# Kernel tuning notes

Hardware: AMD Instinct MI355X
Metric: run time of the kernel (lower is better)

## Reference

```python
import jax, jax.numpy as jnp
import numpy as np

D_MODEL = 1024
NUM_HEADS = 16
DEPTH = D_MODEL // NUM_HEADS
B, S = 2, 2048


def setup_inputs() -> dict:
    key = jax.random.key(0)
    ks = jax.random.split(key, 12)
    std = 1.0 / np.sqrt(D_MODEL)
    inp = {
        "q": jax.random.normal(ks[0], (B, S, D_MODEL), dtype=jnp.float32),
        "k": jax.random.normal(ks[1], (B, S, D_MODEL), dtype=jnp.float32),
        "v": jax.random.normal(ks[2], (B, S, D_MODEL), dtype=jnp.float32),
        "mask": jax.random.randint(ks[3], (B, 1, 1, S), 0, 2, dtype=jnp.int32),
        "wq": jax.random.normal(ks[4], (D_MODEL, D_MODEL), dtype=jnp.float32) * std,
        "bq": jnp.zeros((D_MODEL,), dtype=jnp.float32),
        "wk": jax.random.normal(ks[5], (D_MODEL, D_MODEL), dtype=jnp.float32) * std,
        "bk": jnp.zeros((D_MODEL,), dtype=jnp.float32),
        "wv": jax.random.normal(ks[6], (D_MODEL, D_MODEL), dtype=jnp.float32) * std,
        "bv": jnp.zeros((D_MODEL,), dtype=jnp.float32),
        "wo": jax.random.normal(ks[7], (D_MODEL, D_MODEL), dtype=jnp.float32) * std,
        "bo": jnp.zeros((D_MODEL,), dtype=jnp.float32),
    }
    return inp


def _split_heads(x):
    # (B, S, D) -> (B, H, S, depth)
    b, s, _ = x.shape
    return x.reshape(b, s, NUM_HEADS, DEPTH).transpose(0, 2, 1, 3)


def reference(q, k, v, mask, wq, bq, wk, bk, wv, bv, wo, bo):
    qh = _split_heads(q @ wq + bq)   # (B,H,S,depth)
    kh = _split_heads(k @ wk + bk)
    vh = _split_heads(v @ wv + bv)
    scale = 1.0 / jnp.sqrt(jnp.float32(DEPTH))
    logits = jnp.einsum("bhqd,bhkd->bhqk", qh, kh) * scale  # (B,H,Sq,Sk)
    logits = logits + mask.astype(logits.dtype) * -1e9
    attn = jax.nn.softmax(logits, axis=-1)
    out = jnp.einsum("bhqk,bhkd->bhqd", attn, vh)  # (B,H,Sq,depth)
    out = out.transpose(0, 2, 1, 3).reshape(q.shape[0], -1, D_MODEL)
    return out @ wo + bo
```

## Files before the change

kernel.cpp:

```cpp
#include <hip/hip_runtime.h>
#include <hip/hip_bf16.h>
#include <stdint.h>


typedef __bf16 bf16;
typedef __bf16 bf16x8 __attribute__((ext_vector_type(8)));
typedef __bf16 bf16x4 __attribute__((ext_vector_type(4)));
typedef float  f32x4  __attribute__((ext_vector_type(4)));

#define D_MODEL 1024
#define S_LEN   2048
#define NH      16
#define DEPTH   64

#define LOG2E   1.4426950408889634f
#define QSCALE  (0.125f * LOG2E)
#define SMAX    20.0f
#define PADPEN  (-30000.0f)

__device__ __forceinline__ void gload_lds16(const void* g, void* l) {
  __builtin_amdgcn_global_load_lds(
      (__attribute__((address_space(1))) void*)g,
      (__attribute__((address_space(3))) void*)l,
      16, 0, 0);
}

__global__ __launch_bounds__(256) void setup(
    const void* __restrict__ q, const void* __restrict__ k,
    const void* __restrict__ v, const int* __restrict__ mask,
    const void* __restrict__ wq, const void* __restrict__ wk,
    const void* __restrict__ wv, const void* __restrict__ wo,
    const void* __restrict__ bq, const void* __restrict__ bk,
    const void* __restrict__ bv, const void* __restrict__ bo,
    bf16* __restrict__ wqT, bf16* __restrict__ wkT,
    bf16* __restrict__ wvT, bf16* __restrict__ woT,
    bf16* __restrict__ bqb, bf16* __restrict__ bkb,
    bf16* __restrict__ bvb, bf16* __restrict__ bob,
    bf16* __restrict__ qb, bf16* __restrict__ kb, bf16* __restrict__ vb,
    int* __restrict__ cpos, int* __restrict__ nb, int* __restrict__ flagout)
{
  const int t = threadIdx.x;
  uint32_t w = ((const uint32_t*)q)[t];
  uint32_t e = (w >> 7) & 0xFF;
  int inr = (e >= 90 && e <= 150) ? 1 : 0;
  __shared__ int flg;
  int cnt = __syncthreads_count(inr);
  if (t == 0) flg = (cnt > 160) ? 1 : 0;
  __syncthreads();
  int flag = flg;

  const int bid = blockIdx.x;
  if (bid < 2) {
    const int b = bid;
    const int lane = t & 63, wv4 = t >> 6;
    __shared__ int wsum[4];
    int vals[8], s = 0;
#pragma unroll
    for (int j = 0; j < 8; ++j) {
      vals[j] = (mask[b * S_LEN + t * 8 + j] == 0) ? 1 : 0;
      s += vals[j];
    }
    int acc = s;
    for (int off = 1; off < 64; off <<= 1) {
      int u = __shfl_up(acc, off);
      if (lane >= off) acc += u;
    }
    if (lane == 63) wsum[wv4] = acc;
    __syncthreads();
    int base = 0;
    for (int w4 = 0; w4 < 4; ++w4) base += (w4 < wv4) ? wsum[w4] : 0;
    int ex = base + acc - s;
#pragma unroll
    for (int j = 0; j < 8; ++j) {
      cpos[b * S_LEN + t * 8 + j] = vals[j] ? ex : -1;
      ex += vals[j];
    }
    if (t == 255) nb[b] = base + acc;
    if (b == 0 && t == 0) *flagout = flag;
  } else if (bid < 6) {
    const int j = bid - 2;
    const void* B; bf16* O;
    switch (j) {
      case 0:  B = bq; O = bqb; break;
      case 1:  B = bk; O = bkb; break;
      case 2:  B = bv; O = bvb; break;
      default: B = bo; O = bob; break;
    }
    const float sc = (j == 0) ? QSCALE : 1.0f;
    for (int jj = 0; jj < 4; ++jj) {
      const int i = t + jj * 256;
      const float val = flag ? (float)((const bf16*)B)[i] : ((const float*)B)[i];
      O[i] = (bf16)(val * sc);
    }
  } else if (bid < 6 + 4096) {
    const int job = bid - 6;
    const int wsel = job >> 10, rem = job & 1023;
    const void* W; bf16* T;
    switch (wsel) {
      case 0:  W = wq; T = wqT; break;
      case 1:  W = wk; T = wkT; break;
      case 2:  W = wv; T = wvT; break;
      default: W = wo; T = woT; break;
    }
    const float sc = (wsel == 0) ? QSCALE : 1.0f;
    __shared__ float tile[32][33];
    const int tx = t & 31, ty = t >> 5;
    const int x0 = (rem & 31) * 32;
    const int y0 = (rem >> 5) * 32;
    for (int i = ty; i < 32; i += 8) {
      const size_t gi = (size_t)(y0 + i) * D_MODEL + x0 + tx;
      tile[i][tx] = flag ? (float)((const bf16*)W)[gi] : ((const float*)W)[gi];
    }
    __syncthreads();
    for (int i = ty; i < 32; i += 8)
      T[(size_t)(x0 + i) * D_MODEL + y0 + tx] = (bf16)(tile[tx][i] * sc);
  } else {
    if (flag) return;
    const int job = bid - 4102;
    const int tensor = job >> 11, blk = job & 2047;
    const void* src; bf16* dst;
    switch (tensor) {
      case 0:  src = q; dst = qb; break;
      case 1:  src = k; dst = kb; break;
      default: src = v; dst = vb; break;
    }
    const size_t idx = ((size_t)blk * 256 + t) * 8;
    const float* s = (const float*)src + idx;
    f32x4 a = *(const f32x4*)(s);
    f32x4 b2 = *(const f32x4*)(s + 4);
    bf16x8 o;
    for (int i = 0; i < 4; ++i) { o[i] = (bf16)a[i]; o[4 + i] = (bf16)b2[i]; }
    *(bf16x8*)(dst + idx) = o;
  }
}

struct GArgs {
  const bf16* A;
  const void* Araw;
  const bf16* BT;
  const bf16* bias;
  void* out;
  const int* cpos;
  int mode;
};

__device__ __forceinline__ void gemm_body(const GArgs& g, int flag)
{
  const bf16* A = flag ? (const bf16*)g.Araw : g.A;

  __shared__ __align__(16) bf16 As[2][128 * 32];
  __shared__ __align__(16) bf16 Bs[2][128 * 32];
  const int tid  = threadIdx.x;
  const int wave = tid >> 6, lane = tid & 63;
  const int quad = lane >> 4, l16 = lane & 15;

  const int flat = blockIdx.y * 8 + blockIdx.x;
  const int xcd = flat & 7, pos = flat >> 3;
  const int bx = (xcd & 1) * 4 + (pos & 3);
  const int by = (xcd >> 1) * 8 + (pos >> 2);
  const int m0 = by * 128, n0 = bx * 128;

  const int wm = (wave >> 1) * 64, wn = (wave & 1) * 64;
  const int srow = lane >> 2;
  const int scol = (((lane & 3) ^ ((lane >> 3) & 3)) * 8);

  f32x4 acc[4][4] = {};

  const bf16* Ag = A    + (size_t)(m0 + wave * 32 + srow) * D_MODEL + scol;
  const bf16* Bg = g.BT + (size_t)(n0 + wave * 32 + srow) * D_MODEL + scol;
  const int lbase = (wave * 32) * 32;
  const int rsw = (quad ^ ((l16 >> 1) & 3)) * 8;

  gload_lds16(Ag,                &As[0][lbase]);
  gload_lds16(Ag + 16 * D_MODEL, &As[0][lbase + 16 * 32]);
  gload_lds16(Bg,                &Bs[0][lbase]);
  gload_lds16(Bg + 16 * D_MODEL, &Bs[0][lbase + 16 * 32]);
  __syncthreads();

  int cur = 0;
  for (int kt = 0; kt < D_MODEL; kt += 32, cur ^= 1) {
    if (kt + 32 < D_MODEL) {
      const int nxt = cur ^ 1;
      gload_lds16(Ag + kt + 32,                &As[nxt][lbase]);
      gload_lds16(Ag + kt + 32 + 16 * D_MODEL, &As[nxt][lbase + 16 * 32]);
      gload_lds16(Bg + kt + 32,                &Bs[nxt][lbase]);
      gload_lds16(Bg + kt + 32 + 16 * D_MODEL, &Bs[nxt][lbase + 16 * 32]);
    }

    bf16x8 af[4], bfv[4];
#pragma unroll
    for (int mi = 0; mi < 4; ++mi)
      af[mi] = *(const bf16x8*)(&As[cur][(wm + mi * 16 + l16) * 32 + rsw]);
#pragma unroll
    for (int ni = 0; ni < 4; ++ni)
      bfv[ni] = *(const bf16x8*)(&Bs[cur][(wn + ni * 16 + l16) * 32 + rsw]);
#pragma unroll
    for (int mi = 0; mi < 4; ++mi)
#pragma unroll
      for (int ni = 0; ni < 4; ++ni)
        acc[mi][ni] = __builtin_amdgcn_mfma_f32_16x16x32_bf16(
            af[mi], bfv[ni], acc[mi][ni], 0, 0, 0);

    __syncthreads();
  }

#pragma unroll
  for (int mi = 0; mi < 4; ++mi) {
    const int row0 = m0 + wm + mi * 16 + quad * 4;
    const int b = row0 >> 11, s = row0 & 2047;
    int cp[4];
    if (g.mode >= 2) {
#pragma unroll
      for (int r = 0; r < 4; ++r) cp[r] = g.cpos[b * S_LEN + s + r];
    }
#pragma unroll
    for (int ni = 0; ni < 4; ++ni) {
      const int col  = n0 + wn + ni * 16 + l16;
      const float bv = (float)g.bias[col];
      const int hh = col >> 6, d = col & 63;
      if (g.mode == 3) {
        bf16* base = (bf16*)g.out + (size_t)(b * NH + hh) * S_LEN * DEPTH + d;
#pragma unroll
        for (int r = 0; r < 4; ++r)
          if (cp[r] >= 0) base[(size_t)cp[r] * DEPTH] = (bf16)(acc[mi][ni][r] + bv);
      } else if (g.mode == 2) {
        bf16* base = (bf16*)g.out + ((size_t)(b * NH + hh) * DEPTH + d) * S_LEN;
#pragma unroll
        for (int r = 0; r < 4; ++r)
          if (cp[r] >= 0) base[cp[r]] = (bf16)(acc[mi][ni][r] + bv);
      } else if (g.mode == 1) {
        bf16* op = (bf16*)g.out + ((size_t)(b * NH + hh) * S_LEN + s) * DEPTH + d;
#pragma unroll
        for (int r = 0; r < 4; ++r)
          op[(size_t)r * DEPTH] = (bf16)(acc[mi][ni][r] + bv);
      } else {
        if (flag) {
          bf16* op = (bf16*)g.out + (size_t)row0 * D_MODEL + col;
#pragma unroll
          for (int r = 0; r < 4; ++r)
            op[(size_t)r * D_MODEL] = (bf16)(acc[mi][ni][r] + bv);
        } else {
          float* op = (float*)g.out + (size_t)row0 * D_MODEL + col;
#pragma unroll
          for (int r = 0; r < 4; ++r)
            op[(size_t)r * D_MODEL] = acc[mi][ni][r] + bv;
        }
      }
    }
  }
}

__global__ __launch_bounds__(256) void gemm_qkv(GArgs g0, GArgs g1, GArgs g2,
                                                const int* __restrict__ flagp)
{
  const GArgs& g = (blockIdx.z == 0) ? g0 : ((blockIdx.z == 1) ? g1 : g2);
  gemm_body(g, *flagp);
}

__global__ __launch_bounds__(256) void gemm_out(GArgs g,
                                                const int* __restrict__ flagp)
{
  gemm_body(g, *flagp);
}

__global__ __launch_bounds__(256) void attn(
    const bf16* __restrict__ Qh, const bf16* __restrict__ Kc,
    const bf16* __restrict__ Vc, const int* __restrict__ nbp,
    bf16* __restrict__ Oh)
{
  const int bh = blockIdx.y;
  const int b  = bh >> 4;
  const int h  = bh & 15;
  const int q0 = blockIdx.x * 128;
  const int tid = threadIdx.x, wave = tid >> 6, lane = tid & 63;
  const int quad = lane >> 4, l16 = lane & 15;

  __shared__ __align__(16) bf16 Ks[64][72];
  __shared__ __align__(16) bf16 Vts[64][72];
  __shared__ __align__(16) bf16 Ps[4][32][72];

  const int nbv = nbp[b];
  const int nb_pad = (nbv + 63) & ~63;

  const bf16* Qg = Qh + ((size_t)bh * S_LEN + q0 + wave * 32) * DEPTH;
  bf16x8 aq00 = *(const bf16x8*)(Qg + (size_t)l16 * DEPTH + quad * 8);
  bf16x8 aq01 = *(const bf16x8*)(Qg + (size_t)l16 * DEPTH + 32 + quad * 8);
  bf16x8 aq10 = *(const bf16x8*)(Qg + (size_t)(16 + l16) * DEPTH + quad * 8);
  bf16x8 aq11 = *(const bf16x8*)(Qg + (size_t)(16 + l16) * DEPTH + 32 + quad * 8);

  bf16x8 ones;
#pragma unroll
  for (int j = 0; j < 8; ++j) ones[j] = (bf16)1.0f;

  f32x4 o_acc[2][4] = {};
  f32x4 l_acc[2] = {};

  const bf16* Kg = Kc + (size_t)bh * S_LEN * DEPTH;
  const bf16* Vg = Vc + (size_t)bh * DEPTH * S_LEN;

  const int sr0 = tid >> 3, sc0 = (tid & 7) * 8;
  const int sr1 = sr0 + 32;

  bf16x8 kr0, kr1, vr0, vr1;
  {
    kr0 = *(const bf16x8*)(Kg + (size_t)sr0 * DEPTH + sc0);
    kr1 = *(const bf16x8*)(Kg + (size_t)sr1 * DEPTH + sc0);
    vr0 = *(const bf16x8*)(Vg + (size_t)sr0 * S_LEN + sc0);
    vr1 = *(const bf16x8*)(Vg + (size_t)sr1 * S_LEN + sc0);
  }

  for (int kb = 0; kb < nb_pad; kb += 64) {
    __syncthreads();
    *(bf16x8*)(&Ks[sr0][sc0])  = kr0;
    *(bf16x8*)(&Ks[sr1][sc0])  = kr1;
    *(bf16x8*)(&Vts[sr0][sc0]) = vr0;
    *(bf16x8*)(&Vts[sr1][sc0]) = vr1;
    __syncthreads();
    if (kb + 64 < nb_pad) {
      kr0 = *(const bf16x8*)(Kg + (size_t)(kb + 64 + sr0) * DEPTH + sc0);
      kr1 = *(const bf16x8*)(Kg + (size_t)(kb + 64 + sr1) * DEPTH + sc0);
      vr0 = *(const bf16x8*)(Vg + (size_t)sr0 * S_LEN + kb + 64 + sc0);
      vr1 = *(const bf16x8*)(Vg + (size_t)sr1 * S_LEN + kb + 64 + sc0);
    }

    f32x4 sacc[2][4] = {};
#pragma unroll
    for (int jn = 0; jn < 4; ++jn) {
      bf16x8 bk0 = *(const bf16x8*)(&Ks[jn * 16 + l16][quad * 8]);
      bf16x8 bk1 = *(const bf16x8*)(&Ks[jn * 16 + l16][32 + quad * 8]);
      sacc[0][jn] = __builtin_amdgcn_mfma_f32_16x16x32_bf16(aq00, bk0, sacc[0][jn], 0, 0, 0);
      sacc[0][jn] = __builtin_amdgcn_mfma_f32_16x16x32_bf16(aq01, bk1, sacc[0][jn], 0, 0, 0);
      sacc[1][jn] = __builtin_amdgcn_mfma_f32_16x16x32_bf16(aq10, bk0, sacc[1][jn], 0, 0, 0);
      sacc[1][jn] = __builtin_amdgcn_mfma_f32_16x16x32_bf16(aq11, bk1, sacc[1][jn], 0, 0, 0);
    }

#pragma unroll
    for (int jn = 0; jn < 4; ++jn) {
      const int key = kb + jn * 16 + l16;
      const float pen = (key < nbv) ? (-SMAX) : PADPEN;
#pragma unroll
      for (int qs = 0; qs < 2; ++qs)
#pragma unroll
        for (int r = 0; r < 4; ++r)
          Ps[wave][qs * 16 + quad * 4 + r][jn * 16 + l16] =
              (bf16)__builtin_amdgcn_exp2f(sacc[qs][jn][r] + pen);
    }

    bf16x8 ap00 = *(const bf16x8*)(&Ps[wave][l16][quad * 8]);
    bf16x8 ap01 = *(const bf16x8*)(&Ps[wave][l16][32 + quad * 8]);
    bf16x8 ap10 = *(const bf16x8*)(&Ps[wave][16 + l16][quad * 8]);
    bf16x8 ap11 = *(const bf16x8*)(&Ps[wave][16 + l16][32 + quad * 8]);
#pragma unroll
    for (int jd = 0; jd < 4; ++jd) {
      bf16x8 bv0 = *(const bf16x8*)(&Vts[jd * 16 + l16][quad * 8]);
      bf16x8 bv1 = *(const bf16x8*)(&Vts[jd * 16 + l16][32 + quad * 8]);
      o_acc[0][jd] = __builtin_amdgcn_mfma_f32_16x16x32_bf16(ap00, bv0, o_acc[0][jd], 0, 0, 0);
      o_acc[0][jd] = __builtin_amdgcn_mfma_f32_16x16x32_bf16(ap01, bv1, o_acc[0][jd], 0, 0, 0);
      o_acc[1][jd] = __builtin_amdgcn_mfma_f32_16x16x32_bf16(ap10, bv0, o_acc[1][jd], 0, 0, 0);
      o_acc[1][jd] = __builtin_amdgcn_mfma_f32_16x16x32_bf16(ap11, bv1, o_acc[1][jd], 0, 0, 0);
    }
    l_acc[0] = __builtin_amdgcn_mfma_f32_16x16x32_bf16(ap00, ones, l_acc[0], 0, 0, 0);
    l_acc[0] = __builtin_amdgcn_mfma_f32_16x16x32_bf16(ap01, ones, l_acc[0], 0, 0, 0);
    l_acc[1] = __builtin_amdgcn_mfma_f32_16x16x32_bf16(ap10, ones, l_acc[1], 0, 0, 0);
    l_acc[1] = __builtin_amdgcn_mfma_f32_16x16x32_bf16(ap11, ones, l_acc[1], 0, 0, 0);
  }

#pragma unroll
  for (int qs = 0; qs < 2; ++qs) {
#pragma unroll
    for (int r = 0; r < 4; ++r) {
      const int s = q0 + wave * 32 + qs * 16 + quad * 4 + r;
      const float inv = 1.f / l_acc[qs][r];
#pragma unroll
      for (int jd = 0; jd < 4; ++jd) {
        const int d = jd * 16 + l16;
        Oh[(size_t)(b * S_LEN + s) * D_MODEL + h * DEPTH + d] =
            (bf16)(o_acc[qs][jd][r] * inv);
      }
    }
  }
}

extern "C" void kernel_launch(void* const* d_in, const int* in_sizes, int n_in,
                              void* d_out, int out_size, void* d_ws, size_t ws_size,
                              hipStream_t stream)
{
  const void* q    = d_in[0];
  const void* k    = d_in[1];
  const void* v    = d_in[2];
  const int*  mask = (const int*)d_in[3];
  const void* wq   = d_in[4];
  const void* bq   = d_in[5];
  const void* wk   = d_in[6];
  const void* bk   = d_in[7];
  const void* wv   = d_in[8];
  const void* bv   = d_in[9];
  const void* wo   = d_in[10];
  const void* bo   = d_in[11];

  char* ws = (char*)d_ws;
  const size_t MB = 1u << 20;
  bf16* Qh  = (bf16*)(ws + 0 * MB);
  bf16* Kc  = (bf16*)(ws + 8 * MB);
  bf16* Vc  = (bf16*)(ws + 16 * MB);
  bf16* Oh  = (bf16*)(ws + 24 * MB);
  bf16* wqT = (bf16*)(ws + 32 * MB);
  bf16* wkT = (bf16*)(ws + 34 * MB);
  bf16* wvT = (bf16*)(ws + 36 * MB);
  bf16* woT = (bf16*)(ws + 38 * MB);
  bf16* bqb = (bf16*)(ws + 40 * MB);
  bf16* bkb = (bf16*)(ws + 40 * MB + 4096);
  bf16* bvb = (bf16*)(ws + 40 * MB + 8192);
  bf16* bob = (bf16*)(ws + 40 * MB + 12288);
  int*  flag = (int*)(ws + 40 * MB + 32768);
  int*  cpos = (int*)(ws + 40 * MB + 65536);
  int*  nb   = (int*)(ws + 40 * MB + 65536 + 16384);
  bf16* qb  = (bf16*)(ws + 41 * MB);
  bf16* kb_ = (bf16*)(ws + 49 * MB);
  bf16* vb_ = (bf16*)(ws + 57 * MB);

  setup<<<10246, 256, 0, stream>>>(
      q, k, v, mask, wq, wk, wv, wo, bq, bk, bv, bo,
      wqT, wkT, wvT, woT, bqb, bkb, bvb, bob,
      qb, kb_, vb_, cpos, nb, flag);

  GArgs gq{qb,  q,  wqT, bqb, Qh, nullptr, 1};
  GArgs gk{kb_, k,  wkT, bkb, Kc, cpos,    3};
  GArgs gv{vb_, v,  wvT, bvb, Vc, cpos,    2};
  gemm_qkv<<<dim3(8, 32, 3), 256, 0, stream>>>(gq, gk, gv, flag);

  attn<<<dim3(16, 32), 256, 0, stream>>>(Qh, Kc, Vc, nb, Oh);

  GArgs go{Oh, Oh, woT, bob, d_out, nullptr, 0};
  gemm_out<<<dim3(8, 32), 256, 0, stream>>>(go, flag);
}
```

Measured before the change: 232.0 us.

## Triple-buffer GEMM LDS tiles with prefetch distance two and vmcnt waits

The projection GEMM mainloop moves from a double-buffered LDS scheme to a three-stage ring that prefetches two K-tiles ahead. The full __syncthreads is replaced by an explicit s_waitcnt vmcnt plus s_barrier, so each step waits only for the oldest tile's loads. This lets global-to-LDS loads overlap more with MFMA work and removes a barrier per iteration. In exchange it uses 1.5x the shared memory, which may lower occupancy, and relies on hand-counted vmcnt values being correct.

```diff
diff --git a/kernel.cpp b/kernel.cpp
--- a/kernel.cpp
+++ b/kernel.cpp
@@ -148,8 +148,8 @@
 {
   const bf16* A = flag ? (const bf16*)g.Araw : g.A;
 
-  __shared__ __align__(16) bf16 As[2][128 * 32];
-  __shared__ __align__(16) bf16 Bs[2][128 * 32];
+  __shared__ __align__(16) bf16 As[3][128 * 32];
+  __shared__ __align__(16) bf16 Bs[3][128 * 32];
   const int tid  = threadIdx.x;
   const int wave = tid >> 6, lane = tid & 63;
   const int quad = lane >> 4, l16 = lane & 15;
@@ -171,21 +171,20 @@
   const int lbase = (wave * 32) * 32;
   const int rsw = (quad ^ ((l16 >> 1) & 3)) * 8;
 
-  gload_lds16(Ag,                &As[0][lbase]);
-  gload_lds16(Ag + 16 * D_MODEL, &As[0][lbase + 16 * 32]);
-  gload_lds16(Bg,                &Bs[0][lbase]);
-  gload_lds16(Bg + 16 * D_MODEL, &Bs[0][lbase + 16 * 32]);
-  __syncthreads();
+#pragma unroll
+  for (int p = 0; p < 2; ++p) {
+    gload_lds16(Ag + p * 32,                &As[p][lbase]);
+    gload_lds16(Ag + p * 32 + 16 * D_MODEL, &As[p][lbase + 16 * 32]);
+    gload_lds16(Bg + p * 32,                &Bs[p][lbase]);
+    gload_lds16(Bg + p * 32 + 16 * D_MODEL, &Bs[p][lbase + 16 * 32]);
+  }
 
   int cur = 0;
-  for (int kt = 0; kt < D_MODEL; kt += 32, cur ^= 1) {
-    if (kt + 32 < D_MODEL) {
-      const int nxt = cur ^ 1;
-      gload_lds16(Ag + kt + 32,                &As[nxt][lbase]);
-      gload_lds16(Ag + kt + 32 + 16 * D_MODEL, &As[nxt][lbase + 16 * 32]);
-      gload_lds16(Bg + kt + 32,                &Bs[nxt][lbase]);
-      gload_lds16(Bg + kt + 32 + 16 * D_MODEL, &Bs[nxt][lbase + 16 * 32]);
-    }
+  for (int t = 0; t < 32; ++t) {
+    if (t >= 30) asm volatile("s_waitcnt vmcnt(0)" ::: "memory");
+    else         asm volatile("s_waitcnt vmcnt(4)" ::: "memory");
+    __builtin_amdgcn_s_barrier();
+    __builtin_amdgcn_sched_barrier(0);
 
     bf16x8 af[4], bfv[4];
 #pragma unroll
@@ -201,7 +200,15 @@
         acc[mi][ni] = __builtin_amdgcn_mfma_f32_16x16x32_bf16(
             af[mi], bfv[ni], acc[mi][ni], 0, 0, 0);
 
-    __syncthreads();
+    if (t + 2 < 32) {
+      int nxt = cur + 2; if (nxt >= 3) nxt -= 3;
+      const int kt2 = (t + 2) * 32;
+      gload_lds16(Ag + kt2,                &As[nxt][lbase]);
+      gload_lds16(Ag + kt2 + 16 * D_MODEL, &As[nxt][lbase + 16 * 32]);
+      gload_lds16(Bg + kt2,                &Bs[nxt][lbase]);
+      gload_lds16(Bg + kt2 + 16 * D_MODEL, &Bs[nxt][lbase + 16 * 32]);
+    }
+    cur = (cur == 2) ? 0 : cur + 1;
   }
 
 #pragma unroll
```

After: 240.5 us. +3.6%, slower.
